# Optimization experiments

Hardware: AMD Instinct MI355X
Metric: run time of the kernel (lower is better)

The kernel has to match this reference:

```python
import jax, jax.numpy as jnp
import numpy as np

TEMPERATURE = 0.07
EPS = 1e-8  # torch F.cosine_similarity default eps on the norm product


def setup_inputs() -> dict:
    key = jax.random.key(0)
    k1, k2 = jax.random.split(key)
    emb1 = jax.random.normal(k1, (8192, 128), dtype=jnp.float32)
    emb2 = jax.random.normal(k2, (8192, 128), dtype=jnp.float32)
    return {"emb1": emb1, "emb2": emb2}


def reference(emb1, emb2):
    B1 = emb1.shape[0]
    n1 = jnp.linalg.norm(emb1, axis=1)  # [B1]
    n2 = jnp.linalg.norm(emb2, axis=1)  # [B2]

    # Pairwise cosine similarities via GEMM + clamped norm product (matches F.cosine_similarity eps).
    sim11 = (emb1 @ emb1.T) / jnp.maximum(n1[:, None] * n1[None, :], EPS)  # [B1,B1]
    sim12 = (emb1 @ emb2.T) / jnp.maximum(n1[:, None] * n2[None, :], EPS)  # [B1,B2]

    # loss1 replicates the original loop: for i, for j in [i+1, B1): pair (i, (i+j) % B1).
    I = jnp.arange(B1)[:, None]
    J = jnp.arange(B1)[None, :]
    K = (I + J) % B1                                   # gathered column index
    mask = J > I                                       # j in [i+1, B1)
    vals = jnp.take_along_axis(sim11, K, axis=1)       # sim11[i, (i+j)%B1]
    loss1 = jnp.sum(jnp.where(mask, jnp.exp(vals / TEMPERATURE), 0.0))

    # loss2: all cross pairs between emb1 and emb2.
    loss2 = jnp.sum(jnp.exp(sim12 / TEMPERATURE))

    return (-jnp.log(loss1 / loss2)).reshape(1)
```

## Files before the change

kernel.cpp:

```cpp
#include <hip/hip_runtime.h>

#define B_ROWS   8192
#define BMASK    8191
#define DIM      128
#define CTILE    64
#define CHUNK    16
#define BLK64    16384

typedef __attribute__((ext_vector_type(8)))  __bf16 bf16x8;
typedef __attribute__((ext_vector_type(2)))  __bf16 bf16x2;
typedef __attribute__((ext_vector_type(16))) float  f32x16;

#define RBSCALE 4.5398159f

__device__ __forceinline__ float fast_exp2(float x) {
#if __has_builtin(__builtin_amdgcn_exp2f)
    return __builtin_amdgcn_exp2f(x);
#else
    return exp2f(x);
#endif
}

__global__ __launch_bounds__(256)
void prep_kernel(const float* __restrict__ e1, const float* __restrict__ e2,
                 char* __restrict__ p1, char* __restrict__ p2,
                 float* __restrict__ acc) {
    if (blockIdx.x == 0 && threadIdx.x < 4) acc[threadIdx.x] = 0.f;
    int gw   = (blockIdx.x * 256 + threadIdx.x) >> 6;
    int lane = threadIdx.x & 63;
    const float* src; char* dst; int row;
    if (gw < B_ROWS) { src = e1; dst = p1; row = gw; }
    else             { src = e2; dst = p2; row = gw - B_ROWS; }
    float2 v = ((const float2*)(src + (size_t)row * DIM))[lane];
    float ss = v.x * v.x + v.y * v.y;
#pragma unroll
    for (int o = 32; o > 0; o >>= 1) ss += __shfl_xor(ss, o);
    float rb = RBSCALE / sqrtf(ss);
    bf16x2 pk = { (__bf16)(v.x * rb), (__bf16)(v.y * rb) };
    size_t off = (size_t)(row >> 6) * BLK64 + (size_t)(lane >> 2) * 1024
               + (size_t)(row & 63) * 16 + (size_t)(lane & 3) * 4;
    *(bf16x2*)(dst + off) = pk;
}

template <bool MASKED>
__device__ __forceinline__ float tile_sum(const f32x16& a0, const f32x16& a1,
                                          int i00, int c) {
    float s = 0.f;
#pragma unroll
    for (int g = 0; g < 2; ++g) {
        const f32x16& a = g ? a1 : a0;
        int ib = i00 + g * 32;
#pragma unroll
        for (int r = 0; r < 16; ++r) {
            float ev = fast_exp2(a[r]);
            if (MASKED) {
                int i = ib + (r & 3) + 8 * (r >> 2);
                int d = (c - i) & BMASK;
                s += (d > i) ? ev : 0.f;
            } else {
                s += ev;
            }
        }
    }
    return s;
}

__global__ __launch_bounds__(256, 3)
void pair_kernel(const char* __restrict__ P1, const char* __restrict__ P2,
                 float* __restrict__ accg, float* __restrict__ out,
                 int nz0, int nblocks) {
    __shared__ __align__(16) __bf16 Bbuf[2][8192];
    __shared__ float red[4];

    const int tid  = threadIdx.x;
    const int b    = blockIdx.x;

    int z, p, k0, k1;
    if (b < nz0) {
        z = 0;
        int accb = 0; p = 0;
        for (;; ++p) {
            int i0t = 128 * p;
            int e1t = (i0t > 128) ? i0t : 128;
            int cnt = 2 + (B_ROWS - e1t) / 64;
            int nb  = (cnt + CHUNK - 1) >> 4;
            if (b < accb + nb) {
                int s = b - accb;
                k0 = s * CHUNK;
                k1 = (k0 + CHUNK < cnt) ? (k0 + CHUNK) : cnt;
                break;
            }
            accb += nb;
        }
    } else {
        z = 1;
        int j = b - nz0;
        p = j >> 3;
        k0 = (j & 7) * CHUNK;
        k1 = k0 + CHUNK;
    }
    const int i0 = 128 * p;
    const int e1 = (i0 > 128) ? i0 : 128;

    const char* Bpack = (z == 0) ? P1 : P2;

    auto tile_c0 = [&](int k) -> int {
        if (z) return k * CTILE;
        int e = (k == 0) ? 64 : e1 + (k - 1) * 64;
        return (i0 + e) & BMASK;
    };
    auto tile_masked = [&](int k) -> bool {
        if (z) return false;
        int e = (k == 0) ? 64 : e1 + (k - 1) * 64;
        return (e < i0 + 256) || (e > 8128);
    };

    const int w  = tid >> 6, lane = tid & 63;
    const int w2 = w >> 1, wc = w & 1;
    const int l  = lane & 31, h = lane >> 5;

    bf16x8 af[2][8];
    {
        const char* ap = P1 + (size_t)(p * 2 + w2) * BLK64;
#pragma unroll
        for (int g = 0; g < 2; ++g)
#pragma unroll
            for (int s = 0; s < 8; ++s)
                af[g][s] = *(const bf16x8*)(ap + (size_t)(s * 2 + h) * 1024
                                               + (size_t)(g * 32 + l) * 16);
    }

    auto stage = [&](int bufi, int k) {
        const char* gp = Bpack + (size_t)(tile_c0(k) >> 6) * BLK64 + (size_t)tid * 16;
        char*       lp = (char*)&Bbuf[bufi][0] + (size_t)tid * 16;
#pragma unroll
        for (int r = 0; r < 4; ++r)
            __builtin_amdgcn_global_load_lds(
                (const __attribute__((address_space(1))) unsigned int*)(gp + r * 4096),
                (__attribute__((address_space(3))) unsigned int*)(lp + r * 4096),
                16, 0, 0);
    };

    const int i00 = i0 + w2 * 64 + 4 * h;
    const int cb  = wc * 32 + l;

    float sacc = 0.f;
    stage(0, k0);
    int cur = 0;
    for (int k = k0; k < k1; ++k) {
        __syncthreads();
        if (k + 1 < k1) stage(cur ^ 1, k + 1);

        f32x16 a0, a1;
#pragma unroll
        for (int r = 0; r < 16; ++r) { a0[r] = 0.f; a1[r] = 0.f; }

        const char* bb = (const char*)&Bbuf[cur][0] + (size_t)cb * 16 + (size_t)h * 1024;
#pragma unroll
        for (int s = 0; s < 8; ++s) {
            bf16x8 bf = *(const bf16x8*)(bb + (size_t)s * 2048);
            a0 = __builtin_amdgcn_mfma_f32_32x32x16_bf16(af[0][s], bf, a0, 0, 0, 0);
            a1 = __builtin_amdgcn_mfma_f32_32x32x16_bf16(af[1][s], bf, a1, 0, 0, 0);
        }

        int c = tile_c0(k) + cb;
        sacc += tile_masked(k) ? tile_sum<true >(a0, a1, i00, c)
                               : tile_sum<false>(a0, a1, i00, c);
        cur ^= 1;
    }

#pragma unroll
    for (int o = 32; o > 0; o >>= 1) sacc += __shfl_down(sacc, o);
    if (lane == 0) red[w] = sacc;
    __syncthreads();
    if (tid == 0) {
        atomicAdd(&accg[z], red[0] + red[1] + red[2] + red[3]);
        __threadfence();
        unsigned prev = atomicAdd((unsigned*)&accg[2], 1u);
        if (prev == (unsigned)(nblocks - 1)) {
            float l1 = atomicAdd(&accg[0], 0.f);
            float l2 = atomicAdd(&accg[1], 0.f);
            out[0] = -logf(l1 / l2);
        }
    }
}

extern "C" void kernel_launch(void* const* d_in, const int* in_sizes, int n_in,
                              void* d_out, int out_size, void* d_ws, size_t ws_size,
                              hipStream_t stream) {
    (void)in_sizes; (void)n_in; (void)out_size; (void)ws_size;
    const float* e1 = (const float*)d_in[0];
    const float* e2 = (const float*)d_in[1];
    float* out = (float*)d_out;
    char*  ws  = (char*)d_ws;

    float* acc = (float*)ws;
    char*  p1  = ws + 4096;
    char*  p2  = ws + 4096 + 2097152;

    int nz0 = 0;
    for (int p = 0; p < 64; ++p) {
        int i0 = 128 * p;
        int e1t = (i0 > 128) ? i0 : 128;
        int cnt = 2 + (B_ROWS - e1t) / 64;
        nz0 += (cnt + CHUNK - 1) / CHUNK;
    }
    int nblocks = nz0 + 512;

    prep_kernel<<<dim3(4096), dim3(256), 0, stream>>>(e1, e2, p1, p2, acc);
    pair_kernel<<<dim3(nblocks), dim3(256), 0, stream>>>(p1, p2, acc, out, nz0, nblocks);
}
```

Measured before the change: 112.4 us.

## Halve pair-kernel chunk size, raise occupancy, and vectorize normalization prep

The pair kernel now processes 8 column tiles per block instead of 16, which doubles the block count for both the masked self-similarity part and the cross part, and raises launch_bounds occupancy from 3 to 4 blocks per CU. The prep kernel is restructured so each block handles 64 rows with 4 threads per row, using float4 loads and 16-byte bf16x8 stores instead of one wave per row with 4-byte stores. The exp2 helper now calls exp2f directly rather than the amdgcn builtin. Smaller chunks reduce tail imbalance on the triangular workload but add more per-block A-fragment loads, pipeline prologues and atomics, and exp2f may compile to more instructions.

```diff
diff --git a/kernel.cpp b/kernel.cpp
--- a/kernel.cpp
+++ b/kernel.cpp
@@ -4,21 +4,16 @@
 #define BMASK    8191
 #define DIM      128
 #define CTILE    64
-#define CHUNK    16
+#define CHUNK    8
 #define BLK64    16384
 
 typedef __attribute__((ext_vector_type(8)))  __bf16 bf16x8;
-typedef __attribute__((ext_vector_type(2)))  __bf16 bf16x2;
 typedef __attribute__((ext_vector_type(16))) float  f32x16;
 
 #define RBSCALE 4.5398159f
 
 __device__ __forceinline__ float fast_exp2(float x) {
-#if __has_builtin(__builtin_amdgcn_exp2f)
-    return __builtin_amdgcn_exp2f(x);
-#else
     return exp2f(x);
-#endif
 }
 
 __global__ __launch_bounds__(256)
@@ -26,20 +21,38 @@
                  char* __restrict__ p1, char* __restrict__ p2,
                  float* __restrict__ acc) {
     if (blockIdx.x == 0 && threadIdx.x < 4) acc[threadIdx.x] = 0.f;
-    int gw   = (blockIdx.x * 256 + threadIdx.x) >> 6;
-    int lane = threadIdx.x & 63;
-    const float* src; char* dst; int row;
-    if (gw < B_ROWS) { src = e1; dst = p1; row = gw; }
-    else             { src = e2; dst = p2; row = gw - B_ROWS; }
-    float2 v = ((const float2*)(src + (size_t)row * DIM))[lane];
-    float ss = v.x * v.x + v.y * v.y;
-#pragma unroll
-    for (int o = 32; o > 0; o >>= 1) ss += __shfl_xor(ss, o);
-    float rb = RBSCALE / sqrtf(ss);
-    bf16x2 pk = { (__bf16)(v.x * rb), (__bf16)(v.y * rb) };
-    size_t off = (size_t)(row >> 6) * BLK64 + (size_t)(lane >> 2) * 1024
-               + (size_t)(row & 63) * 16 + (size_t)(lane & 3) * 4;
-    *(bf16x2*)(dst + off) = pk;
+    const int rb = blockIdx.x;
+    const float* src; char* dst; int rb_loc;
+    if (rb < 128) { src = e1; dst = p1; rb_loc = rb; }
+    else          { src = e2; dst = p2; rb_loc = rb - 128; }
+
+    const int t  = threadIdx.x;
+    const int rr = t >> 2;
+    const int q  = t & 3;
+
+    const float* rp = src + (size_t)(rb_loc * 64 + rr) * DIM + q * 32;
+    float4 f[8];
+    float ss = 0.f;
+#pragma unroll
+    for (int j = 0; j < 8; ++j) {
+        f[j] = ((const float4*)rp)[j];
+        ss += f[j].x * f[j].x + f[j].y * f[j].y + f[j].z * f[j].z + f[j].w * f[j].w;
+    }
+    ss += __shfl_xor(ss, 1);
+    ss += __shfl_xor(ss, 2);
+    const float rbn = RBSCALE / sqrtf(ss);
+
+    char* db = dst + (size_t)rb_loc * BLK64;
+#pragma unroll
+    for (int j = 0; j < 4; ++j) {
+        bf16x8 v;
+        float4 a = f[2 * j], b = f[2 * j + 1];
+        v[0] = (__bf16)(a.x * rbn); v[1] = (__bf16)(a.y * rbn);
+        v[2] = (__bf16)(a.z * rbn); v[3] = (__bf16)(a.w * rbn);
+        v[4] = (__bf16)(b.x * rbn); v[5] = (__bf16)(b.y * rbn);
+        v[6] = (__bf16)(b.z * rbn); v[7] = (__bf16)(b.w * rbn);
+        *(bf16x8*)(db + (size_t)(q * 4 + j) * 1024 + (size_t)rr * 16) = v;
+    }
 }
 
 template <bool MASKED>
@@ -65,15 +78,15 @@
     return s;
 }
 
-__global__ __launch_bounds__(256, 3)
+__global__ __launch_bounds__(256, 4)
 void pair_kernel(const char* __restrict__ P1, const char* __restrict__ P2,
                  float* __restrict__ accg, float* __restrict__ out,
                  int nz0, int nblocks) {
     __shared__ __align__(16) __bf16 Bbuf[2][8192];
     __shared__ float red[4];
 
-    const int tid  = threadIdx.x;
-    const int b    = blockIdx.x;
+    const int tid = threadIdx.x;
+    const int b   = blockIdx.x;
 
     int z, p, k0, k1;
     if (b < nz0) {
@@ -83,7 +96,7 @@
             int i0t = 128 * p;
             int e1t = (i0t > 128) ? i0t : 128;
             int cnt = 2 + (B_ROWS - e1t) / 64;
-            int nb  = (cnt + CHUNK - 1) >> 4;
+            int nb  = (cnt + CHUNK - 1) / CHUNK;
             if (b < accb + nb) {
                 int s = b - accb;
                 k0 = s * CHUNK;
@@ -95,8 +108,8 @@
     } else {
         z = 1;
         int j = b - nz0;
-        p = j >> 3;
-        k0 = (j & 7) * CHUNK;
+        p  = j >> 4;
+        k0 = (j & 15) * CHUNK;
         k1 = k0 + CHUNK;
     }
     const int i0 = 128 * p;
@@ -205,8 +218,8 @@
         int cnt = 2 + (B_ROWS - e1t) / 64;
         nz0 += (cnt + CHUNK - 1) / CHUNK;
     }
-    int nblocks = nz0 + 512;
-
-    prep_kernel<<<dim3(4096), dim3(256), 0, stream>>>(e1, e2, p1, p2, acc);
+    int nblocks = nz0 + 1024;
+
+    prep_kernel<<<dim3(256), dim3(256), 0, stream>>>(e1, e2, p1, p2, acc);
     pair_kernel<<<dim3(nblocks), dim3(256), 0, stream>>>(p1, p2, acc, out, nz0, nblocks);
 }
```

Measured after the change: 124.6 us. 10.9% more time.
